# Performance work log

Measured on AMD Instinct MI355X. Metric: run time of the kernel, lower is better.

The kernel has to match this reference:

```python
import jax, jax.numpy as jnp
import numpy as np

Nw, Nt, IN_DIM, OUT_DIM, H, FEAT = 200000, 20000, 128, 256, 8, 64
DH = OUT_DIM // H
DEG = 32
E = Nt * DEG
FFN = 512
NEG_SLOPE = 0.01  # F.leaky_relu default


def setup_inputs() -> dict:
    key = jax.random.key(0)
    ks = jax.random.split(key, 12)
    w = jax.random.normal(ks[0], (Nw, IN_DIM), jnp.float32)
    t = jax.random.normal(ks[1], (Nt, OUT_DIM), jnp.float32)
    topic_feat = jax.random.normal(ks[2], (Nt, FEAT), jnp.float32)
    edge_src = jax.random.randint(ks[3], (E,), 0, Nw)
    # every topic node gets exactly DEG in-edges (sorted dst, no empty segments)
    edge_dst = jnp.repeat(jnp.arange(Nt), DEG)
    s = lambda k, sh, f: jax.random.normal(k, sh, jnp.float32) * np.float32(f)
    fc_w = s(ks[4], (H, IN_DIM, DH), 1.0 / np.sqrt(IN_DIM))
    attn_a = s(ks[5], (H, 2 * DH), 1.0 / np.sqrt(2 * DH))
    dstfeat_w = s(ks[6], (H, FEAT, DH), 1.0 / np.sqrt(FEAT))
    proj_w = s(ks[7], (2 * OUT_DIM, OUT_DIM), 1.0 / np.sqrt(2 * OUT_DIM))
    proj_b = jnp.zeros((OUT_DIM,), jnp.float32)
    ffn_w1 = s(ks[8], (OUT_DIM, FFN), 1.0 / np.sqrt(OUT_DIM))
    ffn_b1 = jnp.zeros((FFN,), jnp.float32)
    ffn_w2 = s(ks[9], (FFN, OUT_DIM), 1.0 / np.sqrt(FFN))
    ffn_b2 = jnp.zeros((OUT_DIM,), jnp.float32)
    ln_scale = jnp.ones((OUT_DIM,), jnp.float32)
    ln_bias = jnp.zeros((OUT_DIM,), jnp.float32)
    return dict(w=w, t=t, topic_feat=topic_feat, edge_src=edge_src, edge_dst=edge_dst,
                fc_w=fc_w, attn_a=attn_a, dstfeat_w=dstfeat_w, proj_w=proj_w, proj_b=proj_b,
                ffn_w1=ffn_w1, ffn_b1=ffn_b1, ffn_w2=ffn_w2, ffn_b2=ffn_b2,
                ln_scale=ln_scale, ln_bias=ln_bias)


def reference(w, t, topic_feat, edge_src, edge_dst, fc_w, attn_a, dstfeat_w,
              proj_w, proj_b, ffn_w1, ffn_b1, ffn_w2, ffn_b2, ln_scale, ln_bias):
    # per-head projections: z on word (src) nodes, dstfeat on topic (dst) nodes
    z = jnp.einsum('ni,hid->hnd', w, fc_w)              # [H, Nw, DH]
    dz = jnp.einsum('nf,hfd->hnd', topic_feat, dstfeat_w)  # [H, Nt, DH]
    # attn_fc(cat(z_src, dstfeat)) decomposes into per-node dot products
    s_src = jnp.einsum('hnd,hd->hn', z, attn_a[:, :DH])   # [H, Nw]
    s_dst = jnp.einsum('hnd,hd->hn', dz, attn_a[:, DH:])  # [H, Nt]
    e = s_src[:, edge_src] + s_dst[:, edge_dst]           # [H, E]
    e = jnp.where(e >= 0, e, NEG_SLOPE * e)               # leaky_relu
    # segment softmax over incoming edges of each dst node (DGL mailbox softmax)
    seg_max = jax.vmap(lambda v: jax.ops.segment_max(v, edge_dst, num_segments=Nt))(e)
    seg_max = jnp.where(jnp.isfinite(seg_max), seg_max, 0.0)  # guard empty segments
    p = jnp.exp(e - seg_max[:, edge_dst])
    denom = jax.vmap(lambda v: jax.ops.segment_sum(v, edge_dst, num_segments=Nt))(p)
    alpha = p / jnp.maximum(denom[:, edge_dst], 1e-9)     # [H, E]
    msg = alpha[:, :, None] * z[:, edge_src, :]           # [H, E, DH]
    agg = jax.vmap(lambda m: jax.ops.segment_sum(m, edge_dst, num_segments=Nt))(msg)  # [H, Nt, DH]
    h = jnp.transpose(agg, (1, 0, 2)).reshape(Nt, OUT_DIM)  # head concat
    h = jax.nn.elu(h)
    h = jnp.concatenate([h, t], axis=-1) @ proj_w + proj_b  # [Nt, OUT_DIM]
    # PositionwiseFeedForward: LN -> gelu -> linear -> residual (dropout off in eval)
    mu = jnp.mean(h, axis=-1, keepdims=True)
    var = jnp.var(h, axis=-1, keepdims=True)
    xn = (h - mu) / jnp.sqrt(var + 1e-6) * ln_scale + ln_bias
    inter = jax.nn.gelu(xn @ ffn_w1 + ffn_b1, approximate=False)
    return (inter @ ffn_w2 + ffn_b2) + h
```

## Files before the change

kernel.cpp:

```cpp
#include <hip/hip_runtime.h>
#include <hip/hip_bf16.h>

typedef __attribute__((ext_vector_type(8))) short short8v;
typedef __attribute__((ext_vector_type(4))) float f32x4;

#define NW 200000
#define NT 20000
#define KIN 128
#define ODIM 256
#define NH 8
#define DH_ 32
#define FEAT_ 64
#define DEG_ 32
#define FFN_ 512
#define NTILE 3125

#define WS_Z     0ull
#define WS_SSRC  102400000ull
#define WS_SDST  108800000ull
#define WS_HBF   109440000ull
#define WS_TBF   119680000ull
#define WS_B1T   129920000ull
#define WS_PWT   129985536ull
#define WS_W1T   130247680ull
#define WS_W2T   130509824ull
#define WS_R1F   130771968ull


__device__ __forceinline__ unsigned short f2bf(float x) {
    __hip_bfloat16 b = __float2bfloat16(x);
    return *reinterpret_cast<unsigned short*>(&b);
}
__device__ __forceinline__ float bf2f(unsigned short u) {
    unsigned int v = ((unsigned int)u) << 16;
    return __uint_as_float(v);
}

__global__ __launch_bounds__(256) void prep_w(const float* __restrict__ fc_w,
        const float* __restrict__ proj_w, const float* __restrict__ w1,
        const float* __restrict__ w2, const float* __restrict__ attn_a,
        unsigned short* __restrict__ b1f, unsigned short* __restrict__ pwf,
        unsigned short* __restrict__ w1f, unsigned short* __restrict__ w2f,
        unsigned short* __restrict__ r1f) {
    int i = blockIdx.x * 256 + threadIdx.x;
    int j = i & 7, l = (i >> 3) & 63;
    int l16 = l & 15, lq = l >> 4;
    if (i < 32768) {
        int kk = (i >> 9) & 3, g = i >> 11;
        int c = g * 16 + l16, k = kk * 32 + lq * 8 + j;
        int h = c >> 5, d = c & 31;
        b1f[i] = f2bf(fc_w[(h * KIN + k) * DH_ + d]);
    }
    if (i < 2048) {
        int kk = i >> 9, s = i & 511;
        int ll = s >> 3, jj = s & 7;
        int c16 = ll & 15, q16 = ll >> 4;
        int k = kk * 32 + q16 * 8 + jj;
        float v = 0.f;
        if (c16 < NH) {
            const float* fw = fc_w + (size_t)(c16 * KIN + k) * DH_;
            const float* aa = attn_a + c16 * 64;
            #pragma unroll
            for (int d = 0; d < DH_; ++d) v += fw[d] * aa[d];
        }
        r1f[i] = f2bf(v);
    }
    {
        int kk = (i >> 9) & 15, g = i >> 13;
        int c = g * 16 + l16, k = kk * 32 + lq * 8 + j;
        int kp = k;
        if (k < 256)
            kp = ((k >> 6) << 6) + (k & 3) * 16 + 2 * ((k >> 3) & 7) + ((k >> 2) & 1);
        pwf[i] = f2bf(proj_w[(size_t)kp * ODIM + c]);
    }
    {
        int kk = (i >> 9) & 7, g = i >> 12;
        int c = g * 16 + l16, k = kk * 32 + lq * 8 + j;
        w1f[i] = f2bf(w1[(size_t)k * FFN_ + c]);
    }
    {
        int kk = (i >> 9) & 15, g = i >> 13;
        int c = g * 16 + l16, k = kk * 32 + lq * 8 + j;
        w2f[i] = f2bf(w2[(size_t)k * ODIM + c]);
    }
}

__global__ __launch_bounds__(256) void prep_t(const float* __restrict__ t,
                                              unsigned short* __restrict__ tbf) {
    int i = blockIdx.x * 256 + threadIdx.x;
    const float4* p = (const float4*)(t + (size_t)i * 8);
    float4 a = p[0], b = p[1];
    short8v o;
    o[0] = (short)f2bf(a.x); o[1] = (short)f2bf(a.y);
    o[2] = (short)f2bf(a.z); o[3] = (short)f2bf(a.w);
    o[4] = (short)f2bf(b.x); o[5] = (short)f2bf(b.y);
    o[6] = (short)f2bf(b.z); o[7] = (short)f2bf(b.w);
    *((short8v*)tbf + i) = o;
}

#define TPB 3
__global__ __launch_bounds__(256) void k1_z(const float* __restrict__ w,
        const unsigned short* __restrict__ b1f, const unsigned short* __restrict__ r1f,
        unsigned short* __restrict__ z, float* __restrict__ s_src) {
    __shared__ unsigned short aS[2][64 * 136];
    const int tid = threadIdx.x;
    const int wv = tid >> 6, l = tid & 63;
    const int l16 = l & 15, lq = l >> 4;
    const int tile0 = blockIdx.x * TPB;
    const int nt = min(TPB, NTILE - tile0);
    float4 vb[8];
    #pragma unroll
    for (int j = 0; j < 8; ++j) {
        int i = tid + j * 256;
        int r = i >> 5, kq = i & 31;
        vb[j] = *(const float4*)(w + (size_t)(tile0 * 64 + r) * KIN + kq * 4);
    }
    #pragma unroll
    for (int j = 0; j < 8; ++j) {
        int i = tid + j * 256;
        int r = i >> 5, kq = i & 31;
        ushort4 u;
        u.x = f2bf(vb[j].x); u.y = f2bf(vb[j].y);
        u.z = f2bf(vb[j].z); u.w = f2bf(vb[j].w);
        *(ushort4*)(&aS[0][r * 136 + kq * 4]) = u;
    }
    for (int t = 0; t < nt; ++t) {
        const int cur = t & 1;
        const int tile = tile0 + t;
        const int row0 = tile * 64;
        if (t < nt - 1) {
            #pragma unroll
            for (int j = 0; j < 8; ++j) {
                int i = tid + j * 256;
                int r = i >> 5, kq = i & 31;
                vb[j] = *(const float4*)(w + (size_t)(row0 + 64 + r) * KIN + kq * 4);
            }
        }
        __syncthreads();
        f32x4 acc[4][4];
        #pragma unroll
        for (int a = 0; a < 4; ++a)
            #pragma unroll
            for (int b = 0; b < 4; ++b)
                acc[a][b] = (f32x4){0.f, 0.f, 0.f, 0.f};
        f32x4 sacc = (f32x4){0.f, 0.f, 0.f, 0.f};
        #pragma unroll
        for (int kk = 0; kk < 4; ++kk) {
            short8v af[4], bfr[4];
            #pragma unroll
            for (int rf = 0; rf < 4; ++rf)
                af[rf] = *(const short8v*)(&aS[cur][(rf * 16 + l16) * 136 + kk * 32 + lq * 8]);
            #pragma unroll
            for (int cf = 0; cf < 4; ++cf)
                bfr[cf] = *(const short8v*)((const short*)b1f +
                            ((((wv * 4 + cf) * 4 + kk) << 9) + l * 8));
            short8v aw = *(const short8v*)(&aS[cur][(wv * 16 + l16) * 136 + kk * 32 + lq * 8]);
            short8v rB = *(const short8v*)((const short*)r1f + ((kk << 9) + l * 8));
            #pragma unroll
            for (int rf = 0; rf < 4; ++rf)
                #pragma unroll
                for (int cf = 0; cf < 4; ++cf)
                    acc[rf][cf] = __builtin_amdgcn_mfma_f32_16x16x32_bf16(
                        af[rf], bfr[cf], acc[rf][cf], 0, 0, 0);
            sacc = __builtin_amdgcn_mfma_f32_16x16x32_bf16(aw, rB, sacc, 0, 0, 0);
        }
        if (l16 < NH) {
            #pragma unroll
            for (int q = 0; q < 4; ++q)
                s_src[(size_t)(row0 + wv * 16 + lq * 4 + q) * NH + l16] = sacc[q];
        }
        #pragma unroll
        for (int rl = 0; rl < 4; ++rl)
            #pragma unroll
            for (int q = 0; q < 4; ++q) {
                ushort4 u;
                u.x = f2bf(acc[rl][0][q]); u.y = f2bf(acc[rl][1][q]);
                u.z = f2bf(acc[rl][2][q]); u.w = f2bf(acc[rl][3][q]);
                ((ushort4*)z)[(size_t)tile * 4096 +
                              (size_t)((((wv * 4 + rl) * 4 + q) * 4 + lq) * 16 + l16)] = u;
            }
        if (t < nt - 1) {
            #pragma unroll
            for (int j = 0; j < 8; ++j) {
                int i = tid + j * 256;
                int r = i >> 5, kq = i & 31;
                ushort4 u;
                u.x = f2bf(vb[j].x); u.y = f2bf(vb[j].y);
                u.z = f2bf(vb[j].z); u.w = f2bf(vb[j].w);
                *(ushort4*)(&aS[cur ^ 1][r * 136 + kq * 4]) = u;
            }
        }
    }
}

__global__ __launch_bounds__(256) void k_sdst(const float* __restrict__ topic_feat,
        const float* __restrict__ dstfeat_w, const float* __restrict__ attn_a,
        float* __restrict__ s_dst) {
    __shared__ float rS[NH * 65];
    __shared__ float tfS[32 * 65];
    const int tid = threadIdx.x;
    for (int i = tid; i < NH * FEAT_; i += 256) {
        int h = i >> 6, f = i & 63;
        const float* dw = dstfeat_w + (size_t)(h * FEAT_ + f) * DH_;
        const float* aa = attn_a + h * 64 + DH_;
        float s = 0.f;
        #pragma unroll
        for (int d = 0; d < DH_; ++d) s += dw[d] * aa[d];
        rS[h * 65 + f] = s;
    }
    const int n0 = blockIdx.x * 32;
    for (int i = tid; i < 32 * FEAT_; i += 256) {
        int n = i >> 6, f = i & 63;
        tfS[n * 65 + f] = topic_feat[(size_t)(n0 + n) * FEAT_ + f];
    }
    __syncthreads();
    int n = tid >> 3, h = tid & 7;
    float s = 0.f;
    #pragma unroll
    for (int f = 0; f < FEAT_; ++f) s += tfS[n * 65 + f] * rS[h * 65 + f];
    s_dst[(size_t)(n0 + n) * NH + h] = s;
}

__global__ __launch_bounds__(256) void k2_attn(const int* __restrict__ edge_src,
        const float* __restrict__ s_src, const float* __restrict__ s_dst,
        const unsigned short* __restrict__ z, unsigned short* __restrict__ hbf) {
    __shared__ int srcS[4][32];
    __shared__ float aS[4][32][8];
    const int tid = threadIdx.x;
    const int nd = tid >> 6, l = tid & 63;
    const int n = blockIdx.x * 4 + nd;
    if (l < 32) srcS[nd][l] = edge_src[(size_t)n * DEG_ + l];
    __syncthreads();
    {
        int e = l & 31, h0 = (l >> 5) * 4;
        int s = srcS[nd][e];
        float4 ss = *(const float4*)(s_src + (size_t)s * NH + h0);
        float4 sd = *(const float4*)(s_dst + (size_t)n * NH + h0);
        float v[4] = {ss.x + sd.x, ss.y + sd.y, ss.z + sd.z, ss.w + sd.w};
        #pragma unroll
        for (int j = 0; j < 4; ++j) v[j] = (v[j] >= 0.f) ? v[j] : 0.01f * v[j];
        float al[4];
        #pragma unroll
        for (int j = 0; j < 4; ++j) {
            float m = v[j];
            #pragma unroll
            for (int off = 16; off >= 1; off >>= 1)
                m = fmaxf(m, __shfl_xor(m, off));
            float p = expf(v[j] - m);
            float su = p;
            #pragma unroll
            for (int off = 16; off >= 1; off >>= 1)
                su += __shfl_xor(su, off);
            al[j] = p / fmaxf(su, 1e-9f);
        }
        float4 a4 = {al[0], al[1], al[2], al[3]};
        *(float4*)(&aS[nd][e][h0]) = a4;
    }
    __syncthreads();
    {
        const int half = l >> 5, cl = l & 31;
        const int wvh = cl >> 3, h0 = wvh * 2;
        const int lo8 = (cl & 7) * 8;
        float acc[8];
        #pragma unroll
        for (int j = 0; j < 8; ++j) acc[j] = 0.f;
        #pragma unroll 4
        for (int ee = 0; ee < 16; ++ee) {
            int e = ee * 2 + half;
            int sp = srcS[nd][e];
            float a_lo = aS[nd][e][h0], a_hi = aS[nd][e][h0 + 1];
            int rr = sp & 63;
            size_t off = (size_t)(sp >> 6) * 16384 +
                (size_t)(((((wvh * 4 + (rr >> 4)) * 4 + (rr & 3)) * 4 + ((rr >> 2) & 3)) * 64) + lo8);
            short8v zv = *(const short8v*)(z + off);
            #pragma unroll
            for (int u = 0; u < 8; ++u) {
                float a = ((u >> 1) & 1) ? a_hi : a_lo;
                acc[u] += a * bf2f((unsigned short)zv[u]);
            }
        }
        #pragma unroll
        for (int j = 0; j < 8; ++j)
            acc[j] += __shfl_xor(acc[j], 32);
        if (half == 0) {
            short8v o;
            #pragma unroll
            for (int j = 0; j < 8; ++j) {
                float v = (acc[j] > 0.f) ? acc[j] : expm1f(acc[j]);
                o[j] = (short)f2bf(v);
            }
            *(short8v*)(hbf + (size_t)n * ODIM + cl * 8) = o;
        }
    }
}

#define BUFP 524
#define XNP  268
__global__ __launch_bounds__(256, 3) void k34_ffn(const unsigned short* __restrict__ hbf,
        const unsigned short* __restrict__ tbf, const unsigned short* __restrict__ pwf,
        const float* __restrict__ proj_b, const float* __restrict__ ln_scale,
        const float* __restrict__ ln_bias, const unsigned short* __restrict__ w1f,
        const float* __restrict__ b1, const unsigned short* __restrict__ w2f,
        const float* __restrict__ b2, float* __restrict__ out) {
    __shared__ unsigned short buf[32 * BUFP];
    __shared__ unsigned short xnS[32 * XNP];
    __shared__ float lnP[4][32], lnQ[4][32];
    __shared__ float muS[32], rsS[32];
    const int tid = threadIdx.x;
    const int row0 = blockIdx.x * 32;
    #pragma unroll
    for (int j = 0; j < 8; ++j) {
        int i = tid + j * 256;
        int r = i >> 6, cq = i & 63;
        ushort4 hv = *(const ushort4*)(hbf + (size_t)(row0 + r) * ODIM + cq * 4);
        *(ushort4*)(&buf[r * BUFP + cq * 4]) = hv;
        ushort4 tv = *(const ushort4*)(tbf + (size_t)(row0 + r) * ODIM + cq * 4);
        *(ushort4*)(&buf[r * BUFP + 256 + cq * 4]) = tv;
    }
    __syncthreads();
    const int wv = tid >> 6, l = tid & 63;
    const int l16 = l & 15, lq = l >> 4;
    const int l8 = l * 8;
    f32x4 acc0[2][4];
    #pragma unroll
    for (int rf = 0; rf < 2; ++rf)
        #pragma unroll
        for (int cf = 0; cf < 4; ++cf) acc0[rf][cf] = (f32x4){0.f, 0.f, 0.f, 0.f};
    {
        short8v bp[2][4];
        #pragma unroll
        for (int cf = 0; cf < 4; ++cf)
            bp[0][cf] = *(const short8v*)((const short*)pwf + ((((wv * 4 + cf) * 16) << 9) + l8));
        #pragma unroll
        for (int kk = 0; kk < 16; ++kk) {
            const int cur = kk & 1;
            if (kk < 15) {
                #pragma unroll
                for (int cf = 0; cf < 4; ++cf)
                    bp[cur ^ 1][cf] = *(const short8v*)((const short*)pwf +
                        ((((wv * 4 + cf) * 16 + kk + 1) << 9) + l8));
            }
            short8v a0 = *(const short8v*)(&buf[l16 * BUFP + kk * 32 + lq * 8]);
            short8v a1 = *(const short8v*)(&buf[(16 + l16) * BUFP + kk * 32 + lq * 8]);
            #pragma unroll
            for (int cf = 0; cf < 4; ++cf) {
                acc0[0][cf] = __builtin_amdgcn_mfma_f32_16x16x32_bf16(a0, bp[cur][cf], acc0[0][cf], 0, 0, 0);
                acc0[1][cf] = __builtin_amdgcn_mfma_f32_16x16x32_bf16(a1, bp[cur][cf], acc0[1][cf], 0, 0, 0);
            }
        }
    }
    #pragma unroll
    for (int cf = 0; cf < 4; ++cf) {
        float bb = proj_b[wv * 64 + cf * 16 + l16];
        #pragma unroll
        for (int rf = 0; rf < 2; ++rf)
            #pragma unroll
            for (int q = 0; q < 4; ++q) acc0[rf][cf][q] += bb;
    }
    #pragma unroll
    for (int rf = 0; rf < 2; ++rf)
        #pragma unroll
        for (int q = 0; q < 4; ++q) {
            float s = 0.f, s2 = 0.f;
            #pragma unroll
            for (int cf = 0; cf < 4; ++cf) {
                float v = acc0[rf][cf][q];
                s += v; s2 += v * v;
            }
            s  += __shfl_xor(s, 1);  s2 += __shfl_xor(s2, 1);
            s  += __shfl_xor(s, 2);  s2 += __shfl_xor(s2, 2);
            s  += __shfl_xor(s, 4);  s2 += __shfl_xor(s2, 4);
            s  += __shfl_xor(s, 8);  s2 += __shfl_xor(s2, 8);
            if (l16 == 0) {
                int row = rf * 16 + lq * 4 + q;
                lnP[wv][row] = s; lnQ[wv][row] = s2;
            }
        }
    __syncthreads();
    if (tid < 32) {
        float s = lnP[0][tid] + lnP[1][tid] + lnP[2][tid] + lnP[3][tid];
        float s2 = lnQ[0][tid] + lnQ[1][tid] + lnQ[2][tid] + lnQ[3][tid];
        float mu = s * (1.f / 256.f);
        float var = s2 * (1.f / 256.f) - mu * mu;
        muS[tid] = mu;
        rsS[tid] = rsqrtf(var + 1e-6f);
    }
    __syncthreads();
    #pragma unroll
    for (int cf = 0; cf < 4; ++cf) {
        int c = wv * 64 + cf * 16 + l16;
        float ls = ln_scale[c], lb = ln_bias[c];
        #pragma unroll
        for (int rf = 0; rf < 2; ++rf)
            #pragma unroll
            for (int q = 0; q < 4; ++q) {
                int row = rf * 16 + lq * 4 + q;
                float x = (acc0[rf][cf][q] - muS[row]) * rsS[row] * ls + lb;
                xnS[row * XNP + c] = f2bf(x);
            }
    }
    __syncthreads();
    {
        f32x4 acc1[2][8];
        #pragma unroll
        for (int rf = 0; rf < 2; ++rf)
            #pragma unroll
            for (int cf = 0; cf < 8; ++cf) acc1[rf][cf] = (f32x4){0.f, 0.f, 0.f, 0.f};
        #pragma unroll 2
        for (int kk = 0; kk < 8; ++kk) {
            short8v a0 = *(const short8v*)(&xnS[l16 * XNP + kk * 32 + lq * 8]);
            short8v a1 = *(const short8v*)(&xnS[(16 + l16) * XNP + kk * 32 + lq * 8]);
            #pragma unroll
            for (int cf = 0; cf < 8; ++cf) {
                short8v b = *(const short8v*)((const short*)w1f +
                    ((((wv * 8 + cf) * 8 + kk) << 9) + l8));
                acc1[0][cf] = __builtin_amdgcn_mfma_f32_16x16x32_bf16(a0, b, acc1[0][cf], 0, 0, 0);
                acc1[1][cf] = __builtin_amdgcn_mfma_f32_16x16x32_bf16(a1, b, acc1[1][cf], 0, 0, 0);
            }
        }
        #pragma unroll
        for (int cf = 0; cf < 8; ++cf) {
            int c = wv * 128 + cf * 16 + l16;
            float bb = b1[c];
            #pragma unroll
            for (int rf = 0; rf < 2; ++rf)
                #pragma unroll
                for (int q = 0; q < 4; ++q) {
                    float x = acc1[rf][cf][q] + bb;
                    x = 0.5f * x * (1.f + erff(x * 0.70710678118654752f));
                    buf[(rf * 16 + lq * 4 + q) * BUFP + c] = f2bf(x);
                }
        }
    }
    __syncthreads();
    {
        f32x4 acc2[2][4];
        #pragma unroll
        for (int rf = 0; rf < 2; ++rf)
            #pragma unroll
            for (int cf = 0; cf < 4; ++cf) acc2[rf][cf] = (f32x4){0.f, 0.f, 0.f, 0.f};
        short8v bp[2][4];
        #pragma unroll
        for (int cf = 0; cf < 4; ++cf)
            bp[0][cf] = *(const short8v*)((const short*)w2f + ((((wv * 4 + cf) * 16) << 9) + l8));
        #pragma unroll
        for (int kk = 0; kk < 16; ++kk) {
            const int cur = kk & 1;
            if (kk < 15) {
                #pragma unroll
                for (int cf = 0; cf < 4; ++cf)
                    bp[cur ^ 1][cf] = *(const short8v*)((const short*)w2f +
                        ((((wv * 4 + cf) * 16 + kk + 1) << 9) + l8));
            }
            short8v a0 = *(const short8v*)(&buf[l16 * BUFP + kk * 32 + lq * 8]);
            short8v a1 = *(const short8v*)(&buf[(16 + l16) * BUFP + kk * 32 + lq * 8]);
            #pragma unroll
            for (int cf = 0; cf < 4; ++cf) {
                acc2[0][cf] = __builtin_amdgcn_mfma_f32_16x16x32_bf16(a0, bp[cur][cf], acc2[0][cf], 0, 0, 0);
                acc2[1][cf] = __builtin_amdgcn_mfma_f32_16x16x32_bf16(a1, bp[cur][cf], acc2[1][cf], 0, 0, 0);
            }
        }
        #pragma unroll
        for (int cf = 0; cf < 4; ++cf) {
            int c = wv * 64 + cf * 16 + l16;
            float bb = b2[c];
            #pragma unroll
            for (int rf = 0; rf < 2; ++rf)
                #pragma unroll
                for (int q = 0; q < 4; ++q) {
                    int row = rf * 16 + lq * 4 + q;
                    out[(size_t)(row0 + row) * ODIM + c] =
                        acc2[rf][cf][q] + bb + acc0[rf][cf][q];
                }
        }
    }
}

extern "C" void kernel_launch(void* const* d_in, const int* in_sizes, int n_in,
                              void* d_out, int out_size, void* d_ws, size_t ws_size,
                              hipStream_t stream) {
    const float* w          = (const float*)d_in[0];
    const float* t          = (const float*)d_in[1];
    const float* topic_feat = (const float*)d_in[2];
    const int*   edge_src   = (const int*)d_in[3];
    const float* fc_w       = (const float*)d_in[5];
    const float* attn_a     = (const float*)d_in[6];
    const float* dstfeat_w  = (const float*)d_in[7];
    const float* proj_w     = (const float*)d_in[8];
    const float* proj_b     = (const float*)d_in[9];
    const float* ffn_w1     = (const float*)d_in[10];
    const float* ffn_b1     = (const float*)d_in[11];
    const float* ffn_w2     = (const float*)d_in[12];
    const float* ffn_b2     = (const float*)d_in[13];
    const float* ln_scale   = (const float*)d_in[14];
    const float* ln_bias    = (const float*)d_in[15];
    float* out = (float*)d_out;

    char* ws = (char*)d_ws;
    unsigned short* z    = (unsigned short*)(ws + WS_Z);
    float* s_src         = (float*)(ws + WS_SSRC);
    float* s_dst         = (float*)(ws + WS_SDST);
    unsigned short* hbf  = (unsigned short*)(ws + WS_HBF);
    unsigned short* tbf  = (unsigned short*)(ws + WS_TBF);
    unsigned short* b1f  = (unsigned short*)(ws + WS_B1T);
    unsigned short* pwf  = (unsigned short*)(ws + WS_PWT);
    unsigned short* w1f  = (unsigned short*)(ws + WS_W1T);
    unsigned short* w2f  = (unsigned short*)(ws + WS_W2T);
    unsigned short* r1f  = (unsigned short*)(ws + WS_R1F);

    hipLaunchKernelGGL(prep_w, dim3(512),  dim3(256), 0, stream,
                       fc_w, proj_w, ffn_w1, ffn_w2, attn_a, b1f, pwf, w1f, w2f, r1f);
    hipLaunchKernelGGL(prep_t, dim3(2500), dim3(256), 0, stream, t, tbf);
    hipLaunchKernelGGL(k1_z,   dim3((NTILE + TPB - 1) / TPB), dim3(256), 0, stream,
                       w, b1f, r1f, z, s_src);
    hipLaunchKernelGGL(k_sdst, dim3(NT / 32), dim3(256), 0, stream,
                       topic_feat, dstfeat_w, attn_a, s_dst);
    hipLaunchKernelGGL(k2_attn, dim3(NT / 4), dim3(256), 0, stream,
                       edge_src, s_src, s_dst, z, hbf);
    hipLaunchKernelGGL(k34_ffn, dim3(NT / 32), dim3(256), 0, stream,
                       hbf, tbf, pwf, proj_b, ln_scale, ln_bias,
                       w1f, ffn_b1, w2f, ffn_b2, out);
}
```

Before: 185.6 us.

## Restructure z projection so each wave owns 16 rows and all columns, dropping LDS staging

The z projection kernel no longer stages 64-row tiles of w in shared memory with a double-buffered multi-tile loop. Each wave now loads its own 16 rows of w directly from global into registers as bf16 fragments. It computes all 256 output columns plus the attention scores for those rows, and the grid becomes one block per 64-row tile. This removes LDS traffic and barriers, but every wave re-reads the full B weight matrix and holds 16 accumulators, which raises register pressure and weight-load traffic.

```diff
diff --git a/kernel.cpp b/kernel.cpp
--- a/kernel.cpp
+++ b/kernel.cpp
@@ -98,99 +98,61 @@
     *((short8v*)tbf + i) = o;
 }
 
-#define TPB 3
 __global__ __launch_bounds__(256) void k1_z(const float* __restrict__ w,
         const unsigned short* __restrict__ b1f, const unsigned short* __restrict__ r1f,
         unsigned short* __restrict__ z, float* __restrict__ s_src) {
-    __shared__ unsigned short aS[2][64 * 136];
     const int tid = threadIdx.x;
     const int wv = tid >> 6, l = tid & 63;
     const int l16 = l & 15, lq = l >> 4;
-    const int tile0 = blockIdx.x * TPB;
-    const int nt = min(TPB, NTILE - tile0);
-    float4 vb[8];
-    #pragma unroll
-    for (int j = 0; j < 8; ++j) {
-        int i = tid + j * 256;
-        int r = i >> 5, kq = i & 31;
-        vb[j] = *(const float4*)(w + (size_t)(tile0 * 64 + r) * KIN + kq * 4);
-    }
-    #pragma unroll
-    for (int j = 0; j < 8; ++j) {
-        int i = tid + j * 256;
-        int r = i >> 5, kq = i & 31;
-        ushort4 u;
-        u.x = f2bf(vb[j].x); u.y = f2bf(vb[j].y);
-        u.z = f2bf(vb[j].z); u.w = f2bf(vb[j].w);
-        *(ushort4*)(&aS[0][r * 136 + kq * 4]) = u;
-    }
-    for (int t = 0; t < nt; ++t) {
-        const int cur = t & 1;
-        const int tile = tile0 + t;
-        const int row0 = tile * 64;
-        if (t < nt - 1) {
-            #pragma unroll
-            for (int j = 0; j < 8; ++j) {
-                int i = tid + j * 256;
-                int r = i >> 5, kq = i & 31;
-                vb[j] = *(const float4*)(w + (size_t)(row0 + 64 + r) * KIN + kq * 4);
-            }
-        }
-        __syncthreads();
-        f32x4 acc[4][4];
-        #pragma unroll
-        for (int a = 0; a < 4; ++a)
-            #pragma unroll
-            for (int b = 0; b < 4; ++b)
-                acc[a][b] = (f32x4){0.f, 0.f, 0.f, 0.f};
+    const int rb = blockIdx.x * 4 + wv;
+    const int tile = rb >> 2, rl = rb & 3;
+    const int row0 = rb * 16;
+    short8v af[4];
+    #pragma unroll
+    for (int kk = 0; kk < 4; ++kk) {
+        const float* wp = w + (size_t)(row0 + l16) * KIN + kk * 32 + lq * 8;
+        float4 v0 = *(const float4*)wp;
+        float4 v1 = *(const float4*)(wp + 4);
+        short8v a;
+        a[0] = (short)f2bf(v0.x); a[1] = (short)f2bf(v0.y);
+        a[2] = (short)f2bf(v0.z); a[3] = (short)f2bf(v0.w);
+        a[4] = (short)f2bf(v1.x); a[5] = (short)f2bf(v1.y);
+        a[6] = (short)f2bf(v1.z); a[7] = (short)f2bf(v1.w);
+        af[kk] = a;
+    }
+    {
         f32x4 sacc = (f32x4){0.f, 0.f, 0.f, 0.f};
         #pragma unroll
         for (int kk = 0; kk < 4; ++kk) {
-            short8v af[4], bfr[4];
-            #pragma unroll
-            for (int rf = 0; rf < 4; ++rf)
-                af[rf] = *(const short8v*)(&aS[cur][(rf * 16 + l16) * 136 + kk * 32 + lq * 8]);
-            #pragma unroll
-            for (int cf = 0; cf < 4; ++cf)
-                bfr[cf] = *(const short8v*)((const short*)b1f +
-                            ((((wv * 4 + cf) * 4 + kk) << 9) + l * 8));
-            short8v aw = *(const short8v*)(&aS[cur][(wv * 16 + l16) * 136 + kk * 32 + lq * 8]);
             short8v rB = *(const short8v*)((const short*)r1f + ((kk << 9) + l * 8));
-            #pragma unroll
-            for (int rf = 0; rf < 4; ++rf)
-                #pragma unroll
-                for (int cf = 0; cf < 4; ++cf)
-                    acc[rf][cf] = __builtin_amdgcn_mfma_f32_16x16x32_bf16(
-                        af[rf], bfr[cf], acc[rf][cf], 0, 0, 0);
-            sacc = __builtin_amdgcn_mfma_f32_16x16x32_bf16(aw, rB, sacc, 0, 0, 0);
+            sacc = __builtin_amdgcn_mfma_f32_16x16x32_bf16(af[kk], rB, sacc, 0, 0, 0);
         }
         if (l16 < NH) {
             #pragma unroll
             for (int q = 0; q < 4; ++q)
-                s_src[(size_t)(row0 + wv * 16 + lq * 4 + q) * NH + l16] = sacc[q];
-        }
-        #pragma unroll
-        for (int rl = 0; rl < 4; ++rl)
-            #pragma unroll
-            for (int q = 0; q < 4; ++q) {
-                ushort4 u;
-                u.x = f2bf(acc[rl][0][q]); u.y = f2bf(acc[rl][1][q]);
-                u.z = f2bf(acc[rl][2][q]); u.w = f2bf(acc[rl][3][q]);
-                ((ushort4*)z)[(size_t)tile * 4096 +
-                              (size_t)((((wv * 4 + rl) * 4 + q) * 4 + lq) * 16 + l16)] = u;
-            }
-        if (t < nt - 1) {
-            #pragma unroll
-            for (int j = 0; j < 8; ++j) {
-                int i = tid + j * 256;
-                int r = i >> 5, kq = i & 31;
-                ushort4 u;
-                u.x = f2bf(vb[j].x); u.y = f2bf(vb[j].y);
-                u.z = f2bf(vb[j].z); u.w = f2bf(vb[j].w);
-                *(ushort4*)(&aS[cur ^ 1][r * 136 + kq * 4]) = u;
-            }
-        }
-    }
+                s_src[(size_t)(row0 + lq * 4 + q) * NH + l16] = sacc[q];
+        }
+    }
+    f32x4 acc[16];
+    #pragma unroll
+    for (int g = 0; g < 16; ++g) acc[g] = (f32x4){0.f, 0.f, 0.f, 0.f};
+    #pragma unroll
+    for (int g = 0; g < 16; ++g)
+        #pragma unroll
+        for (int kk = 0; kk < 4; ++kk) {
+            short8v b = *(const short8v*)((const short*)b1f + (((g * 4 + kk) << 9) + l * 8));
+            acc[g] = __builtin_amdgcn_mfma_f32_16x16x32_bf16(af[kk], b, acc[g], 0, 0, 0);
+        }
+    #pragma unroll
+    for (int wq = 0; wq < 4; ++wq)
+        #pragma unroll
+        for (int q = 0; q < 4; ++q) {
+            ushort4 u;
+            u.x = f2bf(acc[wq * 4 + 0][q]); u.y = f2bf(acc[wq * 4 + 1][q]);
+            u.z = f2bf(acc[wq * 4 + 2][q]); u.w = f2bf(acc[wq * 4 + 3][q]);
+            ((ushort4*)z)[(size_t)tile * 4096 +
+                          (size_t)((((wq * 4 + rl) * 4 + q) * 4 + lq) * 16 + l16)] = u;
+        }
 }
 
 __global__ __launch_bounds__(256) void k_sdst(const float* __restrict__ topic_feat,
@@ -511,7 +473,7 @@
     hipLaunchKernelGGL(prep_w, dim3(512),  dim3(256), 0, stream,
                        fc_w, proj_w, ffn_w1, ffn_w2, attn_a, b1f, pwf, w1f, w2f, r1f);
     hipLaunchKernelGGL(prep_t, dim3(2500), dim3(256), 0, stream, t, tbf);
-    hipLaunchKernelGGL(k1_z,   dim3((NTILE + TPB - 1) / TPB), dim3(256), 0, stream,
+    hipLaunchKernelGGL(k1_z,   dim3(NTILE), dim3(256), 0, stream,
                        w, b1f, r1f, z, s_src);
     hipLaunchKernelGGL(k_sdst, dim3(NT / 32), dim3(256), 0, stream,
                        topic_feat, dstfeat_w, attn_a, s_dst);
```

Result: slower. 224.8 us (+21.1%).
